# Kernel tuning notes

Measured on AMD Instinct MI355X. Metric: run time of the kernel, lower is better.

## Reference

```python
import jax, jax.numpy as jnp
import numpy as np

B, T, N, D = 4, 12, 512, 128
L = 4            # max_lag + 1 lag encoders
H = D // 2       # lag-encoder hidden dim
THRESHOLD = 0.1


def setup_inputs() -> dict:
    key = jax.random.key(0)
    ks = jax.random.split(key, 10)
    s = 0.02
    return {
        "x":   jax.random.normal(ks[0], (B, T, N, D), dtype=jnp.float32),
        # lag encoders: Linear(D->H), ReLU, Linear(H->D), stacked over L lags
        "W1":  s * jax.random.normal(ks[1], (L, D, H), dtype=jnp.float32),
        "b1":  jnp.zeros((L, H), dtype=jnp.float32),
        "W2":  s * jax.random.normal(ks[2], (L, H, D), dtype=jnp.float32),
        "b2":  jnp.zeros((L, D), dtype=jnp.float32),
        # causal scorer: Linear(2D->D), ReLU, (Dropout=id in eval), Linear(D->1), Sigmoid
        "Ws1": s * jax.random.normal(ks[3], (2 * D, D), dtype=jnp.float32),
        "bs1": jnp.zeros((D,), dtype=jnp.float32),
        "Ws2": s * jax.random.normal(ks[4], (D, 1), dtype=jnp.float32),
        "bs2": jnp.zeros((1,), dtype=jnp.float32),
    }


def reference(x, W1, b1, W2, b2, Ws1, bs1, Ws2, bs2):
    Tdim = x.shape[1]
    # lagged slices x[:, T-1-lag] for lag in 0..L-1 (all lags active since T > max_lag)
    lags = jnp.stack([x[:, max(0, Tdim - 1 - l)] for l in range(L)], axis=1)  # (B,L,N,D)
    h = jax.nn.relu(jnp.einsum('blnd,ldh->blnh', lags, W1) + b1[None, :, None, :])
    enc = jnp.einsum('blnh,lhd->blnd', h, W2) + b2[None, :, None, :]          # (B,L,N,D)
    agg = enc.mean(axis=1)                                                    # (B,N,D)

    # pairwise causal scorer. cat([src, tgt]) @ Ws1 == src @ Ws1[:D] + tgt @ Ws1[D:],
    # avoiding the explicit (B,N,N,2D) concat.
    src_proj = jnp.einsum('bnd,dk->bnk', agg, Ws1[:D])   # (B,N,D)
    tgt_proj = jnp.einsum('bnd,dk->bnk', agg, Ws1[D:])   # (B,N,D)
    pre = src_proj[:, :, None, :] + tgt_proj[:, None, :, :] + bs1  # (B,N,N,D)
    score = jax.nn.sigmoid(jnp.einsum('bijd,d->bij', jax.nn.relu(pre), Ws2[:, 0]) + bs2[0])

    # threshold sparsification + remove self loops
    adj = jnp.where(score > THRESHOLD, score, 0.0)
    adj = adj * (1.0 - jnp.eye(N, dtype=adj.dtype))

    # multi-hop propagation and global max normalization per batch element
    a2 = jnp.matmul(adj, adj)
    a3 = jnp.matmul(a2, adj)
    enhanced = adj + 0.5 * a2 + 0.25 * a3
    mx = jnp.max(enhanced, axis=(-1, -2), keepdims=True)
    return enhanced / (mx + 1e-8)
```

## Files before the change

### kernel.cpp

```cpp
#include <hip/hip_runtime.h>
#include <math.h>

#define Bn 4
#define Tn 12
#define Nn 512
#define Dn 128
#define Ln 4
#define Hn 64
#define NNe (Nn*Nn)

typedef __attribute__((ext_vector_type(8))) short short8;
typedef __attribute__((ext_vector_type(4))) float f32x4;

__device__ __forceinline__ unsigned short f2bf(float f) {
    unsigned int u = __float_as_uint(f);
    unsigned int r = (u + 0x7FFF + ((u >> 16) & 1)) >> 16;
    return (unsigned short)r;
}
__device__ __forceinline__ float bf2f(unsigned short s) {
    return __uint_as_float(((unsigned int)s) << 16);
}

__global__ __launch_bounds__(256) void k_enc_a(
    const float* __restrict__ x, const float* __restrict__ W1, const float* __restrict__ b1,
    unsigned short* __restrict__ hb, unsigned int* __restrict__ maxslot)
{
    __shared__ __align__(16) unsigned short xA[32*136];
    __shared__ __align__(16) unsigned short w1T[64*136];
    int tid = threadIdx.x;
    int rg = blockIdx.x, lag = blockIdx.y;
    if (rg == 0 && lag == 0 && tid < Bn) maxslot[tid] = 0u;
    int r0 = rg * 32;
    int bb = r0 >> 9, n0 = r0 & 511;

    {
        const float4* xs = (const float4*)(x + ((size_t)(bb*Tn + (Tn-1-lag))*Nn + n0)*Dn);
        for (int v = tid; v < 1024; v += 256) {
            float4 f = xs[v];
            int row = v >> 5, c4 = v & 31;
            ushort4 o = { f2bf(f.x), f2bf(f.y), f2bf(f.z), f2bf(f.w) };
            *(ushort4*)&xA[row*136 + c4*4] = o;
        }
    }
    {
        int n = tid & 63, kq = tid >> 6;
        const float* Wp = W1 + (size_t)lag*Dn*Hn;
        #pragma unroll
        for (int r = 0; r < 4; ++r) {
            int k0 = (r*4 + kq)*8;
            unsigned short tmp[8];
            #pragma unroll
            for (int j = 0; j < 8; ++j) tmp[j] = f2bf(Wp[(size_t)(k0+j)*Hn + n]);
            *(short8*)&w1T[n*136 + k0] = *(const short8*)tmp;
        }
    }
    __syncthreads();

    int wv = __builtin_amdgcn_readfirstlane(tid >> 6);
    int lane = tid & 63;
    int wm = wv >> 1, wn = wv & 1;
    int m = lane & 15, q = lane >> 4;
    f32x4 acc[2] = {{0.f,0.f,0.f,0.f},{0.f,0.f,0.f,0.f}};
    #pragma unroll
    for (int ks = 0; ks < 4; ++ks) {
        short8 af = *(const short8*)&xA[(wm*16 + m)*136 + ks*32 + q*8];
        #pragma unroll
        for (int nt = 0; nt < 2; ++nt) {
            short8 bg = *(const short8*)&w1T[(wn*32 + nt*16 + m)*136 + ks*32 + q*8];
            acc[nt] = __builtin_amdgcn_mfma_f32_16x16x32_bf16(af, bg, acc[nt], 0, 0, 0);
        }
    }
    int colL = lane & 15, rq = lane >> 4;
    #pragma unroll
    for (int nt = 0; nt < 2; ++nt) {
        int ncol = wn*32 + nt*16 + colL;
        float bv = b1[lag*Hn + ncol];
        #pragma unroll
        for (int reg = 0; reg < 4; ++reg) {
            int rowL = wm*16 + rq*4 + reg;
            hb[(size_t)(r0+rowL)*256 + lag*64 + ncol] = f2bf(fmaxf(acc[nt][reg] + bv, 0.f));
        }
    }
}

__global__ __launch_bounds__(256) void k_enc_b(
    const unsigned short* __restrict__ hb, const float* __restrict__ W2,
    const float* __restrict__ b2, unsigned short* __restrict__ aggb)
{
    __shared__ __align__(16) unsigned short hA[32*264];
    __shared__ __align__(16) unsigned short w2T[64*264];
    int tid = threadIdx.x;
    int rg = blockIdx.x, ch = blockIdx.y;
    int r0 = rg * 32;

    for (int v = tid; v < 1024; v += 256) {
        int row = v >> 5, c = v & 31;
        *(short8*)&hA[row*264 + c*8] = *(const short8*)(hb + (size_t)(r0+row)*256 + c*8);
    }
    {
        int n = tid & 63, kq = tid >> 6;
        #pragma unroll
        for (int r = 0; r < 8; ++r) {
            int k0 = (r*4 + kq)*8;
            unsigned short tmp[8];
            #pragma unroll
            for (int j = 0; j < 8; ++j) tmp[j] = f2bf(W2[(size_t)(k0+j)*Dn + ch*64 + n]);
            *(short8*)&w2T[n*264 + k0] = *(const short8*)tmp;
        }
    }
    __syncthreads();

    int wv = __builtin_amdgcn_readfirstlane(tid >> 6);
    int lane = tid & 63;
    int wm = wv >> 1, wn = wv & 1;
    int m = lane & 15, q = lane >> 4;
    f32x4 acc[2] = {{0.f,0.f,0.f,0.f},{0.f,0.f,0.f,0.f}};
    #pragma unroll
    for (int ks = 0; ks < 8; ++ks) {
        short8 af = *(const short8*)&hA[(wm*16 + m)*264 + ks*32 + q*8];
        #pragma unroll
        for (int nt = 0; nt < 2; ++nt) {
            short8 bg = *(const short8*)&w2T[(wn*32 + nt*16 + m)*264 + ks*32 + q*8];
            acc[nt] = __builtin_amdgcn_mfma_f32_16x16x32_bf16(af, bg, acc[nt], 0, 0, 0);
        }
    }
    int colL = lane & 15, rq = lane >> 4;
    #pragma unroll
    for (int nt = 0; nt < 2; ++nt) {
        int col = ch*64 + wn*32 + nt*16 + colL;
        float b2s = b2[col] + b2[Dn+col] + b2[2*Dn+col] + b2[3*Dn+col];
        #pragma unroll
        for (int reg = 0; reg < 4; ++reg) {
            int rowL = wm*16 + rq*4 + reg;
            aggb[(size_t)(r0+rowL)*Dn + col] = f2bf(0.25f*(acc[nt][reg] + b2s));
        }
    }
}

__global__ __launch_bounds__(256) void k_enc_c(
    const unsigned short* __restrict__ aggb, const float* __restrict__ Ws1,
    const float* __restrict__ bs1,
    unsigned short* __restrict__ spb, unsigned short* __restrict__ tpb)
{
    __shared__ __align__(16) unsigned short aggA[32*136];
    __shared__ __align__(16) unsigned short wsT[128*136];
    int tid = threadIdx.x;
    int rg = blockIdx.x, tgt = blockIdx.y;
    int r0 = rg * 32;

    for (int v = tid; v < 512; v += 256) {
        int row = v >> 4, c = v & 15;
        *(short8*)&aggA[row*136 + c*8] = *(const short8*)(aggb + (size_t)(r0+row)*Dn + c*8);
    }
    {
        int n = tid & 127, kq = tid >> 7;
        #pragma unroll
        for (int r = 0; r < 8; ++r) {
            int k0 = (r*2 + kq)*8;
            unsigned short tmp[8];
            #pragma unroll
            for (int j = 0; j < 8; ++j)
                tmp[j] = f2bf(Ws1[(size_t)(tgt*Dn + k0 + j)*Dn + n]);
            *(short8*)&wsT[n*136 + k0] = *(const short8*)tmp;
        }
    }
    __syncthreads();

    int wv = __builtin_amdgcn_readfirstlane(tid >> 6);
    int lane = tid & 63;
    int wm = wv >> 1, wn = wv & 1;
    int m = lane & 15, q = lane >> 4;
    f32x4 acc[4];
    #pragma unroll
    for (int nt = 0; nt < 4; ++nt) acc[nt] = (f32x4){0.f,0.f,0.f,0.f};
    #pragma unroll
    for (int ks = 0; ks < 4; ++ks) {
        short8 af = *(const short8*)&aggA[(wm*16 + m)*136 + ks*32 + q*8];
        #pragma unroll
        for (int nt = 0; nt < 4; ++nt) {
            short8 bg = *(const short8*)&wsT[(wn*64 + nt*16 + m)*136 + ks*32 + q*8];
            acc[nt] = __builtin_amdgcn_mfma_f32_16x16x32_bf16(af, bg, acc[nt], 0, 0, 0);
        }
    }
    int colL = lane & 15, rq = lane >> 4;
    unsigned short* dst = tgt ? tpb : spb;
    #pragma unroll
    for (int nt = 0; nt < 4; ++nt) {
        int n = wn*64 + nt*16 + colL;
        float bv = tgt ? 0.f : bs1[n];
        #pragma unroll
        for (int reg = 0; reg < 4; ++reg) {
            int rowG = r0 + wm*16 + rq*4 + reg;
            dst[(size_t)rowG*Dn + n] = f2bf(acc[nt][reg] + bv);
        }
    }
}

__global__ __launch_bounds__(256) void k_score(
    const unsigned short* __restrict__ spb, const unsigned short* __restrict__ tpb,
    const float* __restrict__ Ws2, const float* __restrict__ bs2,
    unsigned short* __restrict__ adj_b, unsigned short* __restrict__ adj_bt)
{
    __shared__ float spl[64*132];
    __shared__ unsigned short tplT[Dn*72];
    int tid = threadIdx.x;
    int wv = __builtin_amdgcn_readfirstlane(tid >> 6);
    int lane = tid & 63;
    int bz = blockIdx.z;
    int i0b = blockIdx.y * 64, j0b = blockIdx.x * 64;
    const unsigned short* spr = spb + (size_t)bz*Nn*Dn;
    const unsigned short* tpr = tpb + (size_t)bz*Nn*Dn;

    for (int v = tid; v < 1024; v += 256) {
        int row = v >> 4, c = v & 15;
        const unsigned short* src = spr + (size_t)(i0b+row)*Dn + c*8;
        ushort4 u0 = *(const ushort4*)src;
        ushort4 u1 = *(const ushort4*)(src + 4);
        float4 f0 = { bf2f(u0.x), bf2f(u0.y), bf2f(u0.z), bf2f(u0.w) };
        float4 f1 = { bf2f(u1.x), bf2f(u1.y), bf2f(u1.z), bf2f(u1.w) };
        *(float4*)&spl[row*132 + c*8]     = f0;
        *(float4*)&spl[row*132 + c*8 + 4] = f1;
    }
    {
        int j = tid & 63, kq = tid >> 6;
        for (int p = 0; p < 4; ++p) {
            int k8 = p*4 + kq;
            short8 tv = *(const short8*)(tpr + (size_t)(j0b+j)*Dn + k8*8);
            #pragma unroll
            for (int t = 0; t < 8; ++t) tplT[(k8*8+t)*72 + j] = (unsigned short)tv[t];
        }
    }
    __syncthreads();

    int iq = lane >> 4, jq = lane & 15;
    int iw = wv*16 + iq*4;
    float acc[4][4] = {};
    for (int k8 = 0; k8 < 16; ++k8) {
        float4 wa = *(const float4*)(Ws2 + k8*8);
        float4 wb = *(const float4*)(Ws2 + k8*8 + 4);
        float4 sA[4], sB[4];
        #pragma unroll
        for (int ii = 0; ii < 4; ++ii) {
            sA[ii] = *(const float4*)&spl[(iw+ii)*132 + k8*8];
            sB[ii] = *(const float4*)&spl[(iw+ii)*132 + k8*8 + 4];
        }
        ushort4 t4[8];
        #pragma unroll
        for (int kk = 0; kk < 8; ++kk) t4[kk] = *(const ushort4*)&tplT[(k8*8+kk)*72 + jq*4];
        #pragma unroll
        for (int kk = 0; kk < 8; ++kk) {
            float w = (kk < 4) ? ((const float*)&wa)[kk] : ((const float*)&wb)[kk-4];
            float tv0 = bf2f(t4[kk].x), tv1 = bf2f(t4[kk].y);
            float tv2 = bf2f(t4[kk].z), tv3 = bf2f(t4[kk].w);
            #pragma unroll
            for (int ii = 0; ii < 4; ++ii) {
                float s = (kk < 4) ? ((const float*)&sA[ii])[kk] : ((const float*)&sB[ii])[kk-4];
                acc[ii][0] += fmaxf(s + tv0, 0.f)*w;
                acc[ii][1] += fmaxf(s + tv1, 0.f)*w;
                acc[ii][2] += fmaxf(s + tv2, 0.f)*w;
                acc[ii][3] += fmaxf(s + tv3, 0.f)*w;
            }
        }
    }
    float bsv = bs2[0];
    int i0 = i0b + iw;
    int j0 = j0b + jq*4;
    float vals[4][4];
    #pragma unroll
    for (int ii = 0; ii < 4; ++ii) {
        int i = i0 + ii;
        #pragma unroll
        for (int jj = 0; jj < 4; ++jj) {
            float z = acc[ii][jj] + bsv;
            float sc = 1.f/(1.f + __expf(-z));
            int j = j0 + jj;
            vals[ii][jj] = (sc > 0.1f && i != j) ? sc : 0.f;
        }
    }
    size_t base = (size_t)bz << 18;
    #pragma unroll
    for (int ii = 0; ii < 4; ++ii) {
        ushort4 rv = make_ushort4(f2bf(vals[ii][0]), f2bf(vals[ii][1]),
                                  f2bf(vals[ii][2]), f2bf(vals[ii][3]));
        *(ushort4*)(adj_b + base + (size_t)(i0+ii)*Nn + j0) = rv;
    }
    #pragma unroll
    for (int jj = 0; jj < 4; ++jj) {
        ushort4 cv = make_ushort4(f2bf(vals[0][jj]), f2bf(vals[1][jj]),
                                  f2bf(vals[2][jj]), f2bf(vals[3][jj]));
        *(ushort4*)(adj_bt + base + (size_t)(j0+jj)*Nn + i0) = cv;
    }
}

__global__ __launch_bounds__(256) void k_mm1(
    const unsigned short* __restrict__ adj_b, const unsigned short* __restrict__ adj_bt,
    unsigned short* __restrict__ a2b)
{
    __shared__ unsigned short Als[64*72];
    __shared__ unsigned short Bls[64*72];
    int tid = threadIdx.x;
    int wv = __builtin_amdgcn_readfirstlane(tid >> 6);
    int lane = tid & 63;
    int b = blockIdx.z, i0 = blockIdx.y*64, j0 = blockIdx.x*64;
    size_t base = (size_t)b << 18;
    const unsigned short* Ab = adj_b + base;
    const unsigned short* Bb = adj_bt + base;
    int wm = wv >> 1, wn = wv & 1;
    int m = lane & 15, q = lane >> 4;
    int sr = tid >> 2, sc = (tid & 3)*16;
    f32x4 acc[2][2];
    #pragma unroll
    for (int mt = 0; mt < 2; ++mt)
        #pragma unroll
        for (int nt = 0; nt < 2; ++nt) acc[mt][nt] = (f32x4){0.f,0.f,0.f,0.f};
    short8 pa0, pa1, pb0, pb1;
    pa0 = *(const short8*)(Ab + (size_t)(i0+sr)*Nn + sc);
    pa1 = *(const short8*)(Ab + (size_t)(i0+sr)*Nn + sc + 8);
    pb0 = *(const short8*)(Bb + (size_t)(j0+sr)*Nn + sc);
    pb1 = *(const short8*)(Bb + (size_t)(j0+sr)*Nn + sc + 8);
    for (int kt = 0; kt < 8; ++kt) {
        *(short8*)&Als[sr*72 + sc]     = pa0;
        *(short8*)&Als[sr*72 + sc + 8] = pa1;
        *(short8*)&Bls[sr*72 + sc]     = pb0;
        *(short8*)&Bls[sr*72 + sc + 8] = pb1;
        __syncthreads();
        if (kt < 7) {
            int k0 = (kt+1)*64;
            pa0 = *(const short8*)(Ab + (size_t)(i0+sr)*Nn + k0 + sc);
            pa1 = *(const short8*)(Ab + (size_t)(i0+sr)*Nn + k0 + sc + 8);
            pb0 = *(const short8*)(Bb + (size_t)(j0+sr)*Nn + k0 + sc);
            pb1 = *(const short8*)(Bb + (size_t)(j0+sr)*Nn + k0 + sc + 8);
        }
        #pragma unroll
        for (int ks = 0; ks < 2; ++ks) {
            short8 af[2], bg[2];
            #pragma unroll
            for (int mt = 0; mt < 2; ++mt) af[mt] = *(const short8*)&Als[(wm*32+mt*16+m)*72 + ks*32 + q*8];
            #pragma unroll
            for (int nt = 0; nt < 2; ++nt) bg[nt] = *(const short8*)&Bls[(wn*32+nt*16+m)*72 + ks*32 + q*8];
            #pragma unroll
            for (int mt = 0; mt < 2; ++mt)
                #pragma unroll
                for (int nt = 0; nt < 2; ++nt)
                    acc[mt][nt] = __builtin_amdgcn_mfma_f32_16x16x32_bf16(af[mt], bg[nt], acc[mt][nt], 0, 0, 0);
        }
        __syncthreads();
    }
    int col = lane & 15, rq = lane >> 4;
    #pragma unroll
    for (int mt = 0; mt < 2; ++mt)
        #pragma unroll
        for (int nt = 0; nt < 2; ++nt)
            #pragma unroll
            for (int reg = 0; reg < 4; ++reg) {
                int i = i0 + wm*32 + mt*16 + rq*4 + reg;
                int j = j0 + wn*32 + nt*16 + col;
                a2b[base + (size_t)i*Nn + j] = f2bf(acc[mt][nt][reg]);
            }
}

__global__ __launch_bounds__(256) void k_mm2(
    const unsigned short* __restrict__ adj_b, const unsigned short* __restrict__ adj_bt,
    const unsigned short* __restrict__ a2b,
    float* __restrict__ out, unsigned int* __restrict__ maxslot)
{
    __shared__ unsigned short Als[64*72];
    __shared__ unsigned short Bls[64*72];
    __shared__ float red[4];
    int tid = threadIdx.x;
    int wv = __builtin_amdgcn_readfirstlane(tid >> 6);
    int lane = tid & 63;
    int b = blockIdx.z, i0 = blockIdx.y*64, j0 = blockIdx.x*64;
    size_t base = (size_t)b << 18;
    const unsigned short* Ab = a2b + base;
    const unsigned short* Bb = adj_bt + base;
    int wm = wv >> 1, wn = wv & 1;
    int m = lane & 15, q = lane >> 4;
    int sr = tid >> 2, sc = (tid & 3)*16;
    f32x4 acc[2][2];
    #pragma unroll
    for (int mt = 0; mt < 2; ++mt)
        #pragma unroll
        for (int nt = 0; nt < 2; ++nt) acc[mt][nt] = (f32x4){0.f,0.f,0.f,0.f};
    short8 pa0, pa1, pb0, pb1;
    pa0 = *(const short8*)(Ab + (size_t)(i0+sr)*Nn + sc);
    pa1 = *(const short8*)(Ab + (size_t)(i0+sr)*Nn + sc + 8);
    pb0 = *(const short8*)(Bb + (size_t)(j0+sr)*Nn + sc);
    pb1 = *(const short8*)(Bb + (size_t)(j0+sr)*Nn + sc + 8);
    for (int kt = 0; kt < 8; ++kt) {
        *(short8*)&Als[sr*72 + sc]     = pa0;
        *(short8*)&Als[sr*72 + sc + 8] = pa1;
        *(short8*)&Bls[sr*72 + sc]     = pb0;
        *(short8*)&Bls[sr*72 + sc + 8] = pb1;
        __syncthreads();
        if (kt < 7) {
            int k0 = (kt+1)*64;
            pa0 = *(const short8*)(Ab + (size_t)(i0+sr)*Nn + k0 + sc);
            pa1 = *(const short8*)(Ab + (size_t)(i0+sr)*Nn + k0 + sc + 8);
            pb0 = *(const short8*)(Bb + (size_t)(j0+sr)*Nn + k0 + sc);
            pb1 = *(const short8*)(Bb + (size_t)(j0+sr)*Nn + k0 + sc + 8);
        }
        #pragma unroll
        for (int ks = 0; ks < 2; ++ks) {
            short8 af[2], bg[2];
            #pragma unroll
            for (int mt = 0; mt < 2; ++mt) af[mt] = *(const short8*)&Als[(wm*32+mt*16+m)*72 + ks*32 + q*8];
            #pragma unroll
            for (int nt = 0; nt < 2; ++nt) bg[nt] = *(const short8*)&Bls[(wn*32+nt*16+m)*72 + ks*32 + q*8];
            #pragma unroll
            for (int mt = 0; mt < 2; ++mt)
                #pragma unroll
                for (int nt = 0; nt < 2; ++nt)
                    acc[mt][nt] = __builtin_amdgcn_mfma_f32_16x16x32_bf16(af[mt], bg[nt], acc[mt][nt], 0, 0, 0);
        }
        __syncthreads();
    }
    int col = lane & 15, rq = lane >> 4;
    float lmax = 0.f;
    const unsigned short* adjp = adj_b + base;
    #pragma unroll
    for (int mt = 0; mt < 2; ++mt)
        #pragma unroll
        for (int nt = 0; nt < 2; ++nt)
            #pragma unroll
            for (int reg = 0; reg < 4; ++reg) {
                int i = i0 + wm*32 + mt*16 + rq*4 + reg;
                int j = j0 + wn*32 + nt*16 + col;
                size_t off = (size_t)i*Nn + j;
                float e = bf2f(adjp[off]) + 0.5f*bf2f(Ab[off]) + 0.25f*acc[mt][nt][reg];
                out[base + off] = e;
                lmax = fmaxf(lmax, e);
            }
    #pragma unroll
    for (int s = 1; s < 64; s <<= 1) lmax = fmaxf(lmax, __shfl_xor(lmax, s, 64));
    if (lane == 0) red[wv] = lmax;
    __syncthreads();
    if (tid == 0) {
        float mx = fmaxf(fmaxf(red[0], red[1]), fmaxf(red[2], red[3]));
        atomicMax(maxslot + b, __float_as_uint(mx));
    }
}

__global__ __launch_bounds__(256) void k_norm(float* __restrict__ out,
                                              const unsigned int* __restrict__ maxslot)
{
    int idx = blockIdx.x*256 + threadIdx.x;
    int b = idx >> 16;
    float m = __uint_as_float(maxslot[b]);
    float inv = 1.f/(m + 1e-8f);
    float4* p = (float4*)out + idx;
    float4 v = *p;
    v.x *= inv; v.y *= inv; v.z *= inv; v.w *= inv;
    *p = v;
}

extern "C" void kernel_launch(void* const* d_in, const int* in_sizes, int n_in,
                              void* d_out, int out_size, void* d_ws, size_t ws_size,
                              hipStream_t stream) {
    const float* x   = (const float*)d_in[0];
    const float* W1  = (const float*)d_in[1];
    const float* b1  = (const float*)d_in[2];
    const float* W2  = (const float*)d_in[3];
    const float* b2  = (const float*)d_in[4];
    const float* Ws1 = (const float*)d_in[5];
    const float* bs1 = (const float*)d_in[6];
    const float* Ws2 = (const float*)d_in[7];
    const float* bs2 = (const float*)d_in[8];
    float* out = (float*)d_out;

    unsigned char* wsb = (unsigned char*)d_ws;
    unsigned short* spb    = (unsigned short*)(wsb);
    unsigned short* tpb    = (unsigned short*)(wsb + (512u<<10));
    unsigned short* adj_b  = (unsigned short*)(wsb + (1024u<<10));
    unsigned short* adj_bt = (unsigned short*)(wsb + (3072u<<10));
    unsigned short* a2b    = (unsigned short*)(wsb + (5120u<<10));
    unsigned int*   maxslot= (unsigned int*)(wsb + (7168u<<10));
    unsigned short* hb     = (unsigned short*)(wsb + (7172u<<10));
    unsigned short* aggb   = (unsigned short*)(wsb + (8196u<<10));

    k_enc_a<<<dim3(64, 4),   256, 0, stream>>>(x, W1, b1, hb, maxslot);
    k_enc_b<<<dim3(64, 2),   256, 0, stream>>>(hb, W2, b2, aggb);
    k_enc_c<<<dim3(64, 2),   256, 0, stream>>>(aggb, Ws1, bs1, spb, tpb);
    k_score<<<dim3(8, 8, Bn),256, 0, stream>>>(spb, tpb, Ws2, bs2, adj_b, adj_bt);
    k_mm1  <<<dim3(8, 8, Bn),256, 0, stream>>>(adj_b, adj_bt, a2b);
    k_mm2  <<<dim3(8, 8, Bn),256, 0, stream>>>(adj_b, adj_bt, a2b, out, maxslot);
    k_norm <<<dim3(1024),    256, 0, stream>>>(out, maxslot);
}
```

Baseline: 124.6 us.

## Fuse second lag-encoder GEMM with scorer projections into one kernel

Merges k_enc_b and k_enc_c into a single kernel that keeps the aggregated encoding in shared memory instead of round-tripping it through global memory, saving one launch. Each block now handles 16 rows and loops over output chunks and both projections serially, reloading and converting the weights to bf16 per block. The cost is more serial work per block and repeated weight conversion across 128 blocks, with fewer blocks than the combined grids of the two kernels it replaces.

```diff
diff --git a/kernel.cpp b/kernel.cpp
--- a/kernel.cpp
+++ b/kernel.cpp
@@ -83,115 +83,89 @@
     }
 }
 
-__global__ __launch_bounds__(256) void k_enc_b(
+__global__ __launch_bounds__(256) void k_enc_bc(
     const unsigned short* __restrict__ hb, const float* __restrict__ W2,
-    const float* __restrict__ b2, unsigned short* __restrict__ aggb)
-{
-    __shared__ __align__(16) unsigned short hA[32*264];
-    __shared__ __align__(16) unsigned short w2T[64*264];
+    const float* __restrict__ b2, const float* __restrict__ Ws1,
+    const float* __restrict__ bs1,
+    unsigned short* __restrict__ spb, unsigned short* __restrict__ tpb)
+{
+    __shared__ __align__(16) unsigned short hA[16*264];
+    __shared__ __align__(16) unsigned short wT[64*264];
+    __shared__ __align__(16) unsigned short aggA[16*136];
     int tid = threadIdx.x;
-    int rg = blockIdx.x, ch = blockIdx.y;
-    int r0 = rg * 32;
-
-    for (int v = tid; v < 1024; v += 256) {
+    int wv = __builtin_amdgcn_readfirstlane(tid >> 6);
+    int lane = tid & 63;
+    int r0 = blockIdx.x * 16;
+
+    for (int v = tid; v < 512; v += 256) {
         int row = v >> 5, c = v & 31;
         *(short8*)&hA[row*264 + c*8] = *(const short8*)(hb + (size_t)(r0+row)*256 + c*8);
     }
-    {
-        int n = tid & 63, kq = tid >> 6;
-        #pragma unroll
-        for (int r = 0; r < 8; ++r) {
-            int k0 = (r*4 + kq)*8;
-            unsigned short tmp[8];
-            #pragma unroll
-            for (int j = 0; j < 8; ++j) tmp[j] = f2bf(W2[(size_t)(k0+j)*Dn + ch*64 + n]);
-            *(short8*)&w2T[n*264 + k0] = *(const short8*)tmp;
-        }
-    }
-    __syncthreads();
-
-    int wv = __builtin_amdgcn_readfirstlane(tid >> 6);
-    int lane = tid & 63;
-    int wm = wv >> 1, wn = wv & 1;
+
     int m = lane & 15, q = lane >> 4;
-    f32x4 acc[2] = {{0.f,0.f,0.f,0.f},{0.f,0.f,0.f,0.f}};
-    #pragma unroll
-    for (int ks = 0; ks < 8; ++ks) {
-        short8 af = *(const short8*)&hA[(wm*16 + m)*264 + ks*32 + q*8];
+    int colL = lane & 15, rq = lane >> 4;
+
+    for (int ch = 0; ch < 2; ++ch) {
+        __syncthreads();
+        {
+            int n = tid & 63, kq = tid >> 6;
+            #pragma unroll
+            for (int r = 0; r < 8; ++r) {
+                int k0 = (r*4 + kq)*8;
+                unsigned short tmp[8];
+                #pragma unroll
+                for (int j = 0; j < 8; ++j) tmp[j] = f2bf(W2[(size_t)(k0+j)*Dn + ch*64 + n]);
+                *(short8*)&wT[n*264 + k0] = *(const short8*)tmp;
+            }
+        }
+        __syncthreads();
+        f32x4 acc = {0.f,0.f,0.f,0.f};
+        #pragma unroll
+        for (int ks = 0; ks < 8; ++ks) {
+            short8 af = *(const short8*)&hA[m*264 + ks*32 + q*8];
+            short8 bg = *(const short8*)&wT[(wv*16 + m)*264 + ks*32 + q*8];
+            acc = __builtin_amdgcn_mfma_f32_16x16x32_bf16(af, bg, acc, 0, 0, 0);
+        }
+        int col = ch*64 + wv*16 + colL;
+        float b2s = b2[col] + b2[Dn+col] + b2[2*Dn+col] + b2[3*Dn+col];
+        #pragma unroll
+        for (int reg = 0; reg < 4; ++reg)
+            aggA[(rq*4+reg)*136 + col] = f2bf(0.25f*(acc[reg] + b2s));
+    }
+
+    for (int tgt = 0; tgt < 2; ++tgt) {
+        __syncthreads();
+        {
+            int n = tid & 127, kq = tid >> 7;
+            #pragma unroll
+            for (int r = 0; r < 8; ++r) {
+                int k0 = (r*2 + kq)*8;
+                unsigned short tmp[8];
+                #pragma unroll
+                for (int j = 0; j < 8; ++j)
+                    tmp[j] = f2bf(Ws1[(size_t)(tgt*Dn + k0 + j)*Dn + n]);
+                *(short8*)&wT[n*136 + k0] = *(const short8*)tmp;
+            }
+        }
+        __syncthreads();
+        f32x4 acc[2] = {{0.f,0.f,0.f,0.f},{0.f,0.f,0.f,0.f}};
+        #pragma unroll
+        for (int ks = 0; ks < 4; ++ks) {
+            short8 af = *(const short8*)&aggA[m*136 + ks*32 + q*8];
+            #pragma unroll
+            for (int nt = 0; nt < 2; ++nt) {
+                short8 bg = *(const short8*)&wT[(wv*32 + nt*16 + m)*136 + ks*32 + q*8];
+                acc[nt] = __builtin_amdgcn_mfma_f32_16x16x32_bf16(af, bg, acc[nt], 0, 0, 0);
+            }
+        }
+        unsigned short* dst = tgt ? tpb : spb;
         #pragma unroll
         for (int nt = 0; nt < 2; ++nt) {
-            short8 bg = *(const short8*)&w2T[(wn*32 + nt*16 + m)*264 + ks*32 + q*8];
-            acc[nt] = __builtin_amdgcn_mfma_f32_16x16x32_bf16(af, bg, acc[nt], 0, 0, 0);
-        }
-    }
-    int colL = lane & 15, rq = lane >> 4;
-    #pragma unroll
-    for (int nt = 0; nt < 2; ++nt) {
-        int col = ch*64 + wn*32 + nt*16 + colL;
-        float b2s = b2[col] + b2[Dn+col] + b2[2*Dn+col] + b2[3*Dn+col];
-        #pragma unroll
-        for (int reg = 0; reg < 4; ++reg) {
-            int rowL = wm*16 + rq*4 + reg;
-            aggb[(size_t)(r0+rowL)*Dn + col] = f2bf(0.25f*(acc[nt][reg] + b2s));
-        }
-    }
-}
-
-__global__ __launch_bounds__(256) void k_enc_c(
-    const unsigned short* __restrict__ aggb, const float* __restrict__ Ws1,
-    const float* __restrict__ bs1,
-    unsigned short* __restrict__ spb, unsigned short* __restrict__ tpb)
-{
-    __shared__ __align__(16) unsigned short aggA[32*136];
-    __shared__ __align__(16) unsigned short wsT[128*136];
-    int tid = threadIdx.x;
-    int rg = blockIdx.x, tgt = blockIdx.y;
-    int r0 = rg * 32;
-
-    for (int v = tid; v < 512; v += 256) {
-        int row = v >> 4, c = v & 15;
-        *(short8*)&aggA[row*136 + c*8] = *(const short8*)(aggb + (size_t)(r0+row)*Dn + c*8);
-    }
-    {
-        int n = tid & 127, kq = tid >> 7;
-        #pragma unroll
-        for (int r = 0; r < 8; ++r) {
-            int k0 = (r*2 + kq)*8;
-            unsigned short tmp[8];
-            #pragma unroll
-            for (int j = 0; j < 8; ++j)
-                tmp[j] = f2bf(Ws1[(size_t)(tgt*Dn + k0 + j)*Dn + n]);
-            *(short8*)&wsT[n*136 + k0] = *(const short8*)tmp;
-        }
-    }
-    __syncthreads();
-
-    int wv = __builtin_amdgcn_readfirstlane(tid >> 6);
-    int lane = tid & 63;
-    int wm = wv >> 1, wn = wv & 1;
-    int m = lane & 15, q = lane >> 4;
-    f32x4 acc[4];
-    #pragma unroll
-    for (int nt = 0; nt < 4; ++nt) acc[nt] = (f32x4){0.f,0.f,0.f,0.f};
-    #pragma unroll
-    for (int ks = 0; ks < 4; ++ks) {
-        short8 af = *(const short8*)&aggA[(wm*16 + m)*136 + ks*32 + q*8];
-        #pragma unroll
-        for (int nt = 0; nt < 4; ++nt) {
-            short8 bg = *(const short8*)&wsT[(wn*64 + nt*16 + m)*136 + ks*32 + q*8];
-            acc[nt] = __builtin_amdgcn_mfma_f32_16x16x32_bf16(af, bg, acc[nt], 0, 0, 0);
-        }
-    }
-    int colL = lane & 15, rq = lane >> 4;
-    unsigned short* dst = tgt ? tpb : spb;
-    #pragma unroll
-    for (int nt = 0; nt < 4; ++nt) {
-        int n = wn*64 + nt*16 + colL;
-        float bv = tgt ? 0.f : bs1[n];
-        #pragma unroll
-        for (int reg = 0; reg < 4; ++reg) {
-            int rowG = r0 + wm*16 + rq*4 + reg;
-            dst[(size_t)rowG*Dn + n] = f2bf(acc[nt][reg] + bv);
+            int n = wv*32 + nt*16 + colL;
+            float bv = tgt ? 0.f : bs1[n];
+            #pragma unroll
+            for (int reg = 0; reg < 4; ++reg)
+                dst[(size_t)(r0 + rq*4 + reg)*Dn + n] = f2bf(acc[nt][reg] + bv);
         }
     }
 }
@@ -476,13 +450,11 @@
     unsigned short* a2b    = (unsigned short*)(wsb + (5120u<<10));
     unsigned int*   maxslot= (unsigned int*)(wsb + (7168u<<10));
     unsigned short* hb     = (unsigned short*)(wsb + (7172u<<10));
-    unsigned short* aggb   = (unsigned short*)(wsb + (8196u<<10));
-
-    k_enc_a<<<dim3(64, 4),   256, 0, stream>>>(x, W1, b1, hb, maxslot);
-    k_enc_b<<<dim3(64, 2),   256, 0, stream>>>(hb, W2, b2, aggb);
-    k_enc_c<<<dim3(64, 2),   256, 0, stream>>>(aggb, Ws1, bs1, spb, tpb);
-    k_score<<<dim3(8, 8, Bn),256, 0, stream>>>(spb, tpb, Ws2, bs2, adj_b, adj_bt);
-    k_mm1  <<<dim3(8, 8, Bn),256, 0, stream>>>(adj_b, adj_bt, a2b);
-    k_mm2  <<<dim3(8, 8, Bn),256, 0, stream>>>(adj_b, adj_bt, a2b, out, maxslot);
-    k_norm <<<dim3(1024),    256, 0, stream>>>(out, maxslot);
-}
+
+    k_enc_a <<<dim3(64, 4),   256, 0, stream>>>(x, W1, b1, hb, maxslot);
+    k_enc_bc<<<dim3(128),     256, 0, stream>>>(hb, W2, b2, Ws1, bs1, spb, tpb);
+    k_score <<<dim3(8, 8, Bn),256, 0, stream>>>(spb, tpb, Ws2, bs2, adj_b, adj_bt);
+    k_mm1   <<<dim3(8, 8, Bn),256, 0, stream>>>(adj_b, adj_bt, a2b);
+    k_mm2   <<<dim3(8, 8, Bn),256, 0, stream>>>(adj_b, adj_bt, a2b, out, maxslot);
+    k_norm  <<<dim3(1024),    256, 0, stream>>>(out, maxslot);
+}
```

Result: no change. 123.2 us (median of 2 runs) (-1.2%).
